# Kernel optimization log

Measured on AMD Instinct MI355X. Metric: run time of the kernel, lower is better.

The kernel has to match this reference:

```python
import jax, jax.numpy as jnp
import numpy as np

N = 50000        # nodes
E = 800000       # edges (avg degree 16)
IN = 128         # n_feat
C0, H0 = 32, 4   # layer0: out_channels, heads (concat -> 128)
C1, H1 = 32, 1   # layer1: out_channels, heads (mean)
NEG_SLOPE = 0.2


def setup_inputs() -> dict:
    key = jax.random.key(0)
    ks = jax.random.split(key, 16)
    def p(k, shape, fan):
        return jax.random.normal(k, shape, jnp.float32) / np.float32(np.sqrt(fan))
    x = jax.random.normal(ks[0], (N, IN), jnp.float32)
    edge_index = jax.random.randint(ks[1], (2, E), 0, N, dtype=jnp.int32)
    return {
        "x": x,
        "edge_index": edge_index,
        # layer 0 GATConv: in=128 -> 4 heads x 32, concat
        "W0": p(ks[2], (H0 * C0, IN), IN),
        "att_src0": p(ks[3], (H0, C0), C0),
        "att_dst0": p(ks[4], (H0, C0), C0),
        "bias0": jnp.zeros((H0 * C0,), jnp.float32),
        "linW0": p(ks[5], (H0 * C0, IN), IN),
        "linb0": jnp.zeros((H0 * C0,), jnp.float32),
        # layer 1 GATConv: in=128 -> 1 head x 32, mean
        "W1": p(ks[6], (H1 * C1, H0 * C0), H0 * C0),
        "att_src1": p(ks[7], (H1, C1), C1),
        "att_dst1": p(ks[8], (H1, C1), C1),
        "bias1": jnp.zeros((C1,), jnp.float32),
        "linW1": p(ks[9], (C1, H0 * C0), H0 * C0),
        "linb1": jnp.zeros((C1,), jnp.float32),
    }


def gat_conv(x, src, dst, W, att_src, att_dst, bias, concat):
    """PyG-style GATConv (self-loops already appended to src/dst)."""
    n = x.shape[0]
    H, C = att_src.shape
    h = (x @ W.T).reshape(n, H, C)                       # [N,H,C]
    a_src = jnp.einsum('nhc,hc->nh', h, att_src)          # [N,H]
    a_dst = jnp.einsum('nhc,hc->nh', h, att_dst)          # [N,H]
    e = jax.nn.leaky_relu(a_src[src] + a_dst[dst], NEG_SLOPE)  # [E,H]
    # segment softmax over incoming edges of each dst node
    m = jax.ops.segment_max(e, dst, num_segments=n)       # [N,H]
    ex = jnp.exp(e - m[dst])
    denom = jax.ops.segment_sum(ex, dst, num_segments=n)  # [N,H]
    alpha = ex / (denom[dst] + 1e-16)                     # [E,H]
    out = jax.ops.segment_sum(h[src] * alpha[:, :, None], dst, num_segments=n)  # [N,H,C]
    out = out.reshape(n, H * C) if concat else out.mean(axis=1)
    return out + bias


def reference(x, edge_index, W0, att_src0, att_dst0, bias0, linW0, linb0,
              W1, att_src1, att_dst1, bias1, linW1, linb1):
    n = x.shape[0]
    loop = jnp.arange(n, dtype=edge_index.dtype)
    src = jnp.concatenate([edge_index[0], loop])  # add self-loops
    dst = jnp.concatenate([edge_index[1], loop])
    # layer 0: conv + linear skip, then ELU (eval mode -> dropout is a no-op)
    h = gat_conv(x, src, dst, W0, att_src0, att_dst0, bias0, True) + x @ linW0.T + linb0
    h = jax.nn.elu(h)
    # layer 1 (last): conv + linear skip, no activation
    out = gat_conv(h, src, dst, W1, att_src1, att_dst1, bias1, False) + h @ linW1.T + linb1
    return out
```

## Files before the change

### kernel.cpp

```cpp
#include <hip/hip_runtime.h>
#include <hip/hip_bf16.h>


typedef __attribute__((ext_vector_type(8))) short bf8_t;
typedef __attribute__((ext_vector_type(4))) float f4_t;
typedef __attribute__((ext_vector_type(2))) float f2_t;

#define NBUCK 256
#define BCAP  8192

__device__ inline short f2bf(float f) {
    return (short)__builtin_bit_cast(unsigned short, __float2bfloat16(f));
}
__device__ inline float blo(unsigned int p) { return __uint_as_float(p << 16); }
__device__ inline float bhi(unsigned int p) { return __uint_as_float(p & 0xffff0000u); }
__device__ inline float lrexp(float e) {
    e = (e > 0.f) ? e : 0.2f * e;
    return __expf(e);
}

__global__ __launch_bounds__(256) void k_initbucket(
    const int* __restrict__ ei,
    const float* __restrict__ W0, const float* __restrict__ lW0,
    const float* __restrict__ W1, const float* __restrict__ lW1,
    const float* __restrict__ b0, const float* __restrict__ lb0,
    const float* __restrict__ b1, const float* __restrict__ lb1,
    short* __restrict__ Wp0, short* __restrict__ lWp0,
    short* __restrict__ Wp1, short* __restrict__ lWp1,
    float* __restrict__ bc0, float* __restrict__ bc1,
    int* __restrict__ gcur,
    unsigned int* __restrict__ bucketed, int E, int T) {
    __shared__ int hist[NBUCK];
    __shared__ int gbase[NBUCK];
    int tid = threadIdx.x;

    if (blockIdx.x < 64) {
        int i = blockIdx.x * 256 + tid;
        {
            int j = i & 7, lane = (i >> 3) & 63, kc = i >> 9;
            int kb = kc & 3, ct = kc >> 2;
            int src = (ct * 16 + (lane & 15)) * 128 + kb * 32 + (lane >> 4) * 8 + j;
            Wp0[i]  = f2bf(W0[src]);
            lWp0[i] = f2bf(lW0[src]);
            if (i < 4096) {
                Wp1[i]  = f2bf(W1[src]);
                lWp1[i] = f2bf(lW1[src]);
            }
        }
        if (i < 128) bc0[i] = b0[i] + lb0[i];
        else if (i < 160) bc1[i - 128] = b1[i - 128] + lb1[i - 128];
        return;
    }

    int bb = blockIdx.x - 64;
    hist[tid] = 0;
    __syncthreads();
    int base = bb * 2048;
    unsigned int pk[8]; int rk[8]; int bk[8];
    #pragma unroll
    for (int j = 0; j < 8; j++) {
        int e = base + j * 256 + tid;
        if (e < T) {
            int src, dst;
            if (e < E) { src = ei[e]; dst = ei[E + e]; }
            else       { src = e - E; dst = src; }
            int b = dst >> 8;
            pk[j] = ((unsigned int)dst << 16) | (unsigned int)src;
            bk[j] = b;
            rk[j] = atomicAdd(&hist[b], 1);
        } else bk[j] = -1;
    }
    __syncthreads();
    int h = hist[tid];
    if (h > 0) gbase[tid] = tid * BCAP + atomicAdd(&gcur[tid], h);
    __syncthreads();
    #pragma unroll
    for (int j = 0; j < 8; j++)
        if (bk[j] >= 0)
            bucketed[gbase[bk[j]] + rk[j]] = pk[j];
}


#define TSTR 136

__global__ __launch_bounds__(256) void k_fillgemm0(
    const unsigned int* __restrict__ bucketed, const int* __restrict__ gcur,
    int* __restrict__ rowstart,
    unsigned short* __restrict__ esrc,
    const float* __restrict__ x,
    const short* __restrict__ Wp0, const short* __restrict__ lWp0,
    const float* __restrict__ as0, const float* __restrict__ ad0,
    unsigned char* __restrict__ h0f8, __hip_bfloat16* __restrict__ skipb,
    float* __restrict__ a0s, float* __restrict__ a0d, int N) {
    __shared__ int ihist[256];
    __shared__ int incl[256];
    __shared__ short tile[4][16 * TSTR];
    __shared__ unsigned char t8[4][16 * 136];
    int NBK = (N + 255) >> 8;

    if ((int)blockIdx.x < NBK) {
        int b = blockIdx.x, t = threadIdx.x;
        int nodebase = b << 8;
        int cntt = gcur[t];
        incl[t] = cntt;
        __syncthreads();
        for (int off = 1; off < 256; off <<= 1) {
            int tv = (t >= off) ? incl[t - off] : 0;
            __syncthreads();
            incl[t] += tv;
            __syncthreads();
        }
        int rbase = (b > 0) ? incl[b - 1] : 0;
        if (b == 0 && t == 255) rowstart[N] = incl[255];
        int used = gcur[b];
        const unsigned int* bk = bucketed + (size_t)b * BCAP;
        __syncthreads();
        ihist[t] = 0;
        __syncthreads();
        for (int i = t; i < used; i += 256)
            atomicAdd(&ihist[(bk[i] >> 16) - nodebase], 1);
        __syncthreads();
        int v = ihist[t];
        incl[t] = v;
        __syncthreads();
        for (int off = 1; off < 256; off <<= 1) {
            int tv = (t >= off) ? incl[t - off] : 0;
            __syncthreads();
            incl[t] += tv;
            __syncthreads();
        }
        int myexcl = incl[t] - v;
        int node = nodebase + t;
        if (node < N) rowstart[node] = rbase + myexcl;
        __syncthreads();
        ihist[t] = myexcl;
        __syncthreads();
        for (int i = t; i < used; i += 256) {
            unsigned int p = bk[i];
            int pos = atomicAdd(&ihist[(p >> 16) - nodebase], 1);
            esrc[rbase + pos] = (unsigned short)(p & 0xffffu);
        }
        return;
    }

    int bx = blockIdx.x - NBK;
    int wv = threadIdx.x >> 6, lane = threadIdx.x & 63;
    int rowbase = bx * 64 + wv * 16;
    int m = lane & 15, q = lane >> 4;
    int arow = rowbase + m; if (arow >= N) arow = N - 1;
    bf8_t a[4];
    #pragma unroll
    for (int kb = 0; kb < 4; kb++) {
        const float4* px = (const float4*)(x + (size_t)arow * 128 + kb * 32 + q * 8);
        float4 lo = px[0], hi = px[1];
        bf8_t f;
        f[0] = f2bf(lo.x); f[1] = f2bf(lo.y); f[2] = f2bf(lo.z); f[3] = f2bf(lo.w);
        f[4] = f2bf(hi.x); f[5] = f2bf(hi.y); f[6] = f2bf(hi.z); f[7] = f2bf(hi.w);
        a[kb] = f;
    }
    float sacc[4][4], dacc[4][4];
    #pragma unroll
    for (int h = 0; h < 4; h++)
        #pragma unroll
        for (int r = 0; r < 4; r++) { sacc[h][r] = 0.f; dacc[h][r] = 0.f; }
    short* tl = tile[wv];
    unsigned char* t8l = t8[wv];
    int r4 = lane >> 2, qt = lane & 3;
    int drow = rowbase + r4;

    #pragma unroll
    for (int ct = 0; ct < 8; ct++) {
        f4_t acc = {0.f, 0.f, 0.f, 0.f};
        #pragma unroll
        for (int kb = 0; kb < 4; kb++) {
            bf8_t b = *(const bf8_t*)(Wp0 + (((ct * 4 + kb) * 64 + lane) << 3));
            acc = __builtin_amdgcn_mfma_f32_16x16x32_bf16(a[kb], b, acc, 0, 0, 0);
        }
        int hd = ct >> 1;
        float ws = as0[ct * 16 + m], wd = ad0[ct * 16 + m];
        #pragma unroll
        for (int r = 0; r < 4; r++) {
            sacc[hd][r] += acc[r] * ws;
            dacc[hd][r] += acc[r] * wd;
            int pk8 = __builtin_amdgcn_cvt_pk_fp8_f32(acc[r], acc[r], 0, false);
            t8l[(q * 4 + r) * 136 + ct * 16 + m] = (unsigned char)(pk8 & 0xff);
        }
    }
    if (drow < N) {
        const unsigned char* sp8 = t8l + r4 * 136 + qt * 32;
        uint2 w0 = ((const uint2*)sp8)[0];
        uint2 w1 = ((const uint2*)sp8)[1];
        uint2 w2 = ((const uint2*)sp8)[2];
        uint2 w3 = ((const uint2*)sp8)[3];
        uint4 o0 = make_uint4(w0.x, w0.y, w1.x, w1.y);
        uint4 o1 = make_uint4(w2.x, w2.y, w3.x, w3.y);
        unsigned char* dst = h0f8 + (size_t)drow * 128 + qt * 32;
        *(uint4*)dst = o0;
        *(uint4*)(dst + 16) = o1;
    }

    #pragma unroll
    for (int ct = 0; ct < 8; ct++) {
        f4_t acc = {0.f, 0.f, 0.f, 0.f};
        #pragma unroll
        for (int kb = 0; kb < 4; kb++) {
            bf8_t b = *(const bf8_t*)(lWp0 + (((ct * 4 + kb) * 64 + lane) << 3));
            acc = __builtin_amdgcn_mfma_f32_16x16x32_bf16(a[kb], b, acc, 0, 0, 0);
        }
        #pragma unroll
        for (int r = 0; r < 4; r++)
            tl[(q * 4 + r) * TSTR + ct * 16 + m] = f2bf(acc[r]);
    }
    if (drow < N) {
        short* dst = (short*)skipb + (size_t)drow * 128 + qt * 32;
        const short* srcp = tl + r4 * TSTR + qt * 32;
        #pragma unroll
        for (int s = 0; s < 4; s++)
            *(uint4*)(dst + s * 8) = *(const uint4*)(srcp + s * 8);
    }

    #pragma unroll
    for (int h = 0; h < 4; h++)
        #pragma unroll
        for (int r = 0; r < 4; r++) {
            float s = sacc[h][r], d = dacc[h][r];
            #pragma unroll
            for (int off = 1; off < 16; off <<= 1) {
                s += __shfl_xor(s, off);
                d += __shfl_xor(d, off);
            }
            sacc[h][r] = s; dacc[h][r] = d;
        }
    if (m < 4) {
        #pragma unroll
        for (int r = 0; r < 4; r++) {
            int row = rowbase + q * 4 + r;
            if (row < N) {
                float sv = (m == 0) ? sacc[0][r] : (m == 1) ? sacc[1][r]
                         : (m == 2) ? sacc[2][r] : sacc[3][r];
                float dv = (m == 0) ? dacc[0][r] : (m == 1) ? dacc[1][r]
                         : (m == 2) ? dacc[2][r] : dacc[3][r];
                a0s[row * 4 + m] = sv;
                a0d[row * 4 + m] = dv;
            }
        }
    }
}


__global__ __launch_bounds__(256) void k_aggfuse(
    const int* __restrict__ rowstart, const unsigned short* __restrict__ esrc,
    const uint2* __restrict__ h0f8,
    const float* __restrict__ a0s, const float* __restrict__ a0d,
    const float* __restrict__ bc0,
    const unsigned int* __restrict__ skip0,
    const short* __restrict__ Wp1, const short* __restrict__ lWp1,
    const float* __restrict__ as1, const float* __restrict__ ad1,
    __hip_bfloat16* __restrict__ h1, float* __restrict__ outskip,
    float* __restrict__ a1s, float* __restrict__ a1d, int n) {
    __shared__ __align__(16) short hrow[16][136];
    __shared__ __align__(16) short th[16 * 40];
    __shared__ __align__(16) float ts[16 * 36];
    __shared__ float satt[2][16], datt[2][16];

    int tid = threadIdx.x;
    int nl = tid >> 4, t = tid & 15, hd = t >> 2;
    int rowbase = blockIdx.x << 4;
    int node = rowbase + nl;

    if (node < n) {
        float ad = a0d[node * 4 + hd];
        int s0 = rowstart[node], s1 = rowstart[node + 1];
        float den = 0.f;
        float acc[8];
        #pragma unroll
        for (int k = 0; k < 8; k++) acc[k] = 0.f;
        int i = s0;
        for (; i + 3 < s1; i += 4) {
            int sE[4]; float e[4]; uint2 p[4];
            #pragma unroll
            for (int j = 0; j < 4; j++) sE[j] = esrc[i + j];
            #pragma unroll
            for (int j = 0; j < 4; j++) e[j] = a0s[sE[j] * 4 + hd] + ad;
            #pragma unroll
            for (int j = 0; j < 4; j++) p[j] = h0f8[(size_t)sE[j] * 16 + t];
            #pragma unroll
            for (int j = 0; j < 4; j++) {
                float wgt = lrexp(e[j]);
                den += wgt;
                f2_t c01 = __builtin_amdgcn_cvt_pk_f32_fp8(p[j].x, false);
                f2_t c23 = __builtin_amdgcn_cvt_pk_f32_fp8(p[j].x, true);
                f2_t c45 = __builtin_amdgcn_cvt_pk_f32_fp8(p[j].y, false);
                f2_t c67 = __builtin_amdgcn_cvt_pk_f32_fp8(p[j].y, true);
                acc[0] += wgt * c01.x; acc[1] += wgt * c01.y;
                acc[2] += wgt * c23.x; acc[3] += wgt * c23.y;
                acc[4] += wgt * c45.x; acc[5] += wgt * c45.y;
                acc[6] += wgt * c67.x; acc[7] += wgt * c67.y;
            }
        }
        for (; i < s1; ++i) {
            int s = esrc[i];
            float wgt = lrexp(a0s[s * 4 + hd] + ad);
            uint2 p = h0f8[(size_t)s * 16 + t];
            den += wgt;
            f2_t c01 = __builtin_amdgcn_cvt_pk_f32_fp8(p.x, false);
            f2_t c23 = __builtin_amdgcn_cvt_pk_f32_fp8(p.x, true);
            f2_t c45 = __builtin_amdgcn_cvt_pk_f32_fp8(p.y, false);
            f2_t c67 = __builtin_amdgcn_cvt_pk_f32_fp8(p.y, true);
            acc[0] += wgt * c01.x; acc[1] += wgt * c01.y;
            acc[2] += wgt * c23.x; acc[3] += wgt * c23.y;
            acc[4] += wgt * c45.x; acc[5] += wgt * c45.y;
            acc[6] += wgt * c67.x; acc[7] += wgt * c67.y;
        }
        float inv = 1.0f / (den + 1e-16f);
        uint4 sp = *(const uint4*)(skip0 + (size_t)node * 64 + t * 4);
        int c0 = t * 8;
        float o[8];
        o[0] = acc[0] * inv + blo(sp.x) + bc0[c0 + 0];
        o[1] = acc[1] * inv + bhi(sp.x) + bc0[c0 + 1];
        o[2] = acc[2] * inv + blo(sp.y) + bc0[c0 + 2];
        o[3] = acc[3] * inv + bhi(sp.y) + bc0[c0 + 3];
        o[4] = acc[4] * inv + blo(sp.z) + bc0[c0 + 4];
        o[5] = acc[5] * inv + bhi(sp.z) + bc0[c0 + 5];
        o[6] = acc[6] * inv + blo(sp.w) + bc0[c0 + 6];
        o[7] = acc[7] * inv + bhi(sp.w) + bc0[c0 + 7];
        #pragma unroll
        for (int k = 0; k < 8; k++)
            o[k] = (o[k] > 0.f) ? o[k] : (__expf(o[k]) - 1.f);
        uint4 res;
        res.x = (unsigned int)(unsigned short)f2bf(o[0]) | ((unsigned int)(unsigned short)f2bf(o[1]) << 16);
        res.y = (unsigned int)(unsigned short)f2bf(o[2]) | ((unsigned int)(unsigned short)f2bf(o[3]) << 16);
        res.z = (unsigned int)(unsigned short)f2bf(o[4]) | ((unsigned int)(unsigned short)f2bf(o[5]) << 16);
        res.w = (unsigned int)(unsigned short)f2bf(o[6]) | ((unsigned int)(unsigned short)f2bf(o[7]) << 16);
        *(uint4*)&hrow[nl][t * 8] = res;
    } else {
        *(uint4*)&hrow[nl][t * 8] = make_uint4(0u, 0u, 0u, 0u);
    }
    __syncthreads();

    int wv = tid >> 6, lane = tid & 63;
    int m = lane & 15, q = lane >> 4;
    bf8_t a[4];
    #pragma unroll
    for (int kb = 0; kb < 4; kb++)
        a[kb] = *(const bf8_t*)&hrow[m][kb * 32 + q * 8];
    int ct = wv & 1;
    const short* Wt = (wv < 2) ? Wp1 : lWp1;
    f4_t acc = {0.f, 0.f, 0.f, 0.f};
    #pragma unroll
    for (int kb = 0; kb < 4; kb++) {
        bf8_t b = *(const bf8_t*)(Wt + (((ct * 4 + kb) * 64 + lane) << 3));
        acc = __builtin_amdgcn_mfma_f32_16x16x32_bf16(a[kb], b, acc, 0, 0, 0);
    }
    if (wv < 2) {
        float wsv = as1[ct * 16 + m], wdv = ad1[ct * 16 + m];
        #pragma unroll
        for (int r = 0; r < 4; r++) {
            th[(q * 4 + r) * 40 + ct * 16 + m] = f2bf(acc[r]);
            float s = acc[r] * wsv, d = acc[r] * wdv;
            #pragma unroll
            for (int off = 1; off < 16; off <<= 1) {
                s += __shfl_xor(s, off);
                d += __shfl_xor(d, off);
            }
            if (m == 0) { satt[ct][q * 4 + r] = s; datt[ct][q * 4 + r] = d; }
        }
    } else {
        #pragma unroll
        for (int r = 0; r < 4; r++)
            ts[(q * 4 + r) * 36 + ct * 16 + m] = acc[r];
    }
    __syncthreads();

    if (tid < 64) {
        int row = tid >> 2, qt = tid & 3;
        if (rowbase + row < n)
            *(uint4*)((short*)h1 + (size_t)(rowbase + row) * 32 + qt * 8) =
                *(const uint4*)&th[row * 40 + qt * 8];
    } else if (tid < 192) {
        int i2 = tid - 64, row = i2 >> 3, qt = i2 & 7;
        if (rowbase + row < n)
            *(uint4*)(outskip + (size_t)(rowbase + row) * 32 + qt * 4) =
                *(const uint4*)&ts[row * 36 + qt * 4];
    } else if (tid < 208) {
        int r2 = tid - 192;
        if (rowbase + r2 < n) {
            a1s[rowbase + r2] = satt[0][r2] + satt[1][r2];
            a1d[rowbase + r2] = datt[0][r2] + datt[1][r2];
        }
    }
}


__global__ __launch_bounds__(256) void k_agg1(
    const int* __restrict__ rowstart, const unsigned short* __restrict__ esrc,
    const __hip_bfloat16* __restrict__ h1,
    const float* __restrict__ a1s, const float* __restrict__ a1d,
    const float* __restrict__ bc1,
    float* __restrict__ out, int n) {
    int node = (blockIdx.x * 256 + threadIdx.x) >> 6;
    int lane = threadIdx.x & 63;
    if (node >= n) return;
    int g = lane >> 4, t = lane & 15;
    float ad = a1d[node];
    int s0 = rowstart[node], s1 = rowstart[node + 1];
    const unsigned int* h1w = (const unsigned int*)h1;
    float den = 0.f, acc0 = 0.f, acc1 = 0.f;
    int i = s0 + g;
    for (; i + 12 < s1; i += 16) {
        int sE[4]; float e[4]; unsigned int p[4];
        #pragma unroll
        for (int j = 0; j < 4; j++) sE[j] = esrc[i + 4 * j];
        #pragma unroll
        for (int j = 0; j < 4; j++) e[j] = a1s[sE[j]] + ad;
        #pragma unroll
        for (int j = 0; j < 4; j++) p[j] = h1w[(size_t)sE[j] * 16 + t];
        #pragma unroll
        for (int j = 0; j < 4; j++) {
            float wgt = lrexp(e[j]);
            den += wgt;
            acc0 += wgt * blo(p[j]);
            acc1 += wgt * bhi(p[j]);
        }
    }
    for (; i < s1; i += 4) {
        int s = esrc[i];
        float wv = lrexp(a1s[s] + ad);
        unsigned int p = h1w[(size_t)s * 16 + t];
        den += wv; acc0 += wv * blo(p); acc1 += wv * bhi(p);
    }
    acc0 += __shfl_xor(acc0, 16); acc0 += __shfl_xor(acc0, 32);
    acc1 += __shfl_xor(acc1, 16); acc1 += __shfl_xor(acc1, 32);
    den  += __shfl_xor(den, 16);  den  += __shfl_xor(den, 32);
    if (g == 0) {
        float inv = 1.0f / (den + 1e-16f);
        int c0 = t * 2;
        size_t idx = (size_t)node * 32 + c0;
        float2 sk = *(const float2*)(out + idx);
        float2 r;
        r.x = acc0 * inv + sk.x + bc1[c0];
        r.y = acc1 * inv + sk.y + bc1[c0 + 1];
        *(float2*)(out + idx) = r;
    }
}


extern "C" void kernel_launch(void* const* d_in, const int* in_sizes, int n_in,
                              void* d_out, int out_size, void* d_ws, size_t ws_size,
                              hipStream_t stream) {
    const float* x   = (const float*)d_in[0];
    const int*   ei  = (const int*)d_in[1];
    const float* W0  = (const float*)d_in[2];
    const float* as0 = (const float*)d_in[3];
    const float* ad0 = (const float*)d_in[4];
    const float* b0  = (const float*)d_in[5];
    const float* lW0 = (const float*)d_in[6];
    const float* lb0 = (const float*)d_in[7];
    const float* W1  = (const float*)d_in[8];
    const float* as1 = (const float*)d_in[9];
    const float* ad1 = (const float*)d_in[10];
    const float* b1  = (const float*)d_in[11];
    const float* lW1 = (const float*)d_in[12];
    const float* lb1 = (const float*)d_in[13];
    float* out = (float*)d_out;

    const int N = in_sizes[0] / 128;
    const int E = in_sizes[1] / 2;
    const int T = E + N;
    const int NBK  = (N + 255) >> 8;
    const int NBBK = (T + 2047) / 2048;

    char* w = (char*)d_ws;
    auto alloc = [&](size_t bytes) -> char* {
        char* p = w; w += (bytes + 255) / 256 * 256; return p;
    };
    int* rowstart  = (int*)alloc((size_t)(N + 1) * 4);
    int* gcur      = (int*)alloc(NBUCK * 4);
    unsigned int* bucketed = (unsigned int*)alloc((size_t)NBUCK * BCAP * 4);
    unsigned short* esrc = (unsigned short*)alloc((size_t)T * 2);
    float* aS      = (float*)alloc((size_t)N * 4 * 4);
    float* aD      = (float*)alloc((size_t)N * 4 * 4);
    char* hbuf     = alloc((size_t)N * 128);
    __hip_bfloat16* skip0 = (__hip_bfloat16*)alloc((size_t)N * 128 * 2);
    __hip_bfloat16* h1buf = (__hip_bfloat16*)alloc((size_t)N * 32 * 2);
    float* aS1     = (float*)alloc((size_t)N * 4);
    float* aD1     = (float*)alloc((size_t)N * 4);
    short* Wp0  = (short*)alloc(16384 * 2);
    short* lWp0 = (short*)alloc(16384 * 2);
    short* Wp1  = (short*)alloc(4096 * 2);
    short* lWp1 = (short*)alloc(4096 * 2);
    float* bc0  = (float*)alloc(128 * 4);
    float* bc1  = (float*)alloc(32 * 4);

    hipMemsetAsync(gcur, 0, NBUCK * sizeof(int), stream);
    k_initbucket<<<64 + NBBK, 256, 0, stream>>>(ei, W0, lW0, W1, lW1,
                                                b0, lb0, b1, lb1,
                                                Wp0, lWp0, Wp1, lWp1, bc0, bc1,
                                                gcur, bucketed, E, T);
    k_fillgemm0<<<NBK + (N + 63) / 64, 256, 0, stream>>>(
        bucketed, gcur, rowstart, esrc,
        x, Wp0, lWp0, as0, ad0, (unsigned char*)hbuf, skip0, aS, aD, N);
    k_aggfuse<<<(N + 15) / 16, 256, 0, stream>>>(
        rowstart, esrc, (const uint2*)hbuf, aS, aD, bc0,
        (const unsigned int*)skip0, Wp1, lWp1, as1, ad1,
        h1buf, out, aS1, aD1, N);
    k_agg1<<<(N + 3) / 4, 256, 0, stream>>>(rowstart, esrc, h1buf,
                                            aS1, aD1, bc1, out, N);
}
```

Baseline: 187.6 us.

## Merge four kernels and memset into one persistent cooperative kernel with grid syncs

Replaces the memset plus four separate kernel launches with a single cooperative persistent kernel. The blocks loop over virtual block indices for each stage and use grid.sync between stages. Shared memory is overlaid in one raw buffer. The goal is to remove launch overhead and inter-kernel gaps. The cost is lower occupancy, grid-sync barriers and a grid sized by occupancy queries.

```diff
diff --git a/kernel.cpp b/kernel.cpp
--- a/kernel.cpp
+++ b/kernel.cpp
@@ -1,5 +1,8 @@
 #include <hip/hip_runtime.h>
 #include <hip/hip_bf16.h>
+#include <hip/hip_cooperative_groups.h>
+
+namespace cg = cooperative_groups;
 
 
 typedef __attribute__((ext_vector_type(8))) short bf8_t;
@@ -8,6 +11,7 @@
 
 #define NBUCK 256
 #define BCAP  8192
+#define TSTR  136
 
 __device__ inline short f2bf(float f) {
     return (short)__builtin_bit_cast(unsigned short, __float2bfloat16(f));
@@ -19,491 +23,488 @@
     return __expf(e);
 }
 
-__global__ __launch_bounds__(256) void k_initbucket(
-    const int* __restrict__ ei,
-    const float* __restrict__ W0, const float* __restrict__ lW0,
-    const float* __restrict__ W1, const float* __restrict__ lW1,
-    const float* __restrict__ b0, const float* __restrict__ lb0,
-    const float* __restrict__ b1, const float* __restrict__ lb1,
-    short* __restrict__ Wp0, short* __restrict__ lWp0,
-    short* __restrict__ Wp1, short* __restrict__ lWp1,
-    float* __restrict__ bc0, float* __restrict__ bc1,
-    int* __restrict__ gcur,
-    unsigned int* __restrict__ bucketed, int E, int T) {
-    __shared__ int hist[NBUCK];
-    __shared__ int gbase[NBUCK];
-    int tid = threadIdx.x;
-
-    if (blockIdx.x < 64) {
-        int i = blockIdx.x * 256 + tid;
-        {
-            int j = i & 7, lane = (i >> 3) & 63, kc = i >> 9;
-            int kb = kc & 3, ct = kc >> 2;
-            int src = (ct * 16 + (lane & 15)) * 128 + kb * 32 + (lane >> 4) * 8 + j;
-            Wp0[i]  = f2bf(W0[src]);
-            lWp0[i] = f2bf(lW0[src]);
-            if (i < 4096) {
-                Wp1[i]  = f2bf(W1[src]);
-                lWp1[i] = f2bf(lW1[src]);
-            }
-        }
-        if (i < 128) bc0[i] = b0[i] + lb0[i];
-        else if (i < 160) bc1[i - 128] = b1[i - 128] + lb1[i - 128];
-        return;
-    }
-
-    int bb = blockIdx.x - 64;
-    hist[tid] = 0;
-    __syncthreads();
-    int base = bb * 2048;
-    unsigned int pk[8]; int rk[8]; int bk[8];
-    #pragma unroll
-    for (int j = 0; j < 8; j++) {
-        int e = base + j * 256 + tid;
-        if (e < T) {
-            int src, dst;
-            if (e < E) { src = ei[e]; dst = ei[E + e]; }
-            else       { src = e - E; dst = src; }
-            int b = dst >> 8;
-            pk[j] = ((unsigned int)dst << 16) | (unsigned int)src;
-            bk[j] = b;
-            rk[j] = atomicAdd(&hist[b], 1);
-        } else bk[j] = -1;
-    }
-    __syncthreads();
-    int h = hist[tid];
-    if (h > 0) gbase[tid] = tid * BCAP + atomicAdd(&gcur[tid], h);
-    __syncthreads();
-    #pragma unroll
-    for (int j = 0; j < 8; j++)
-        if (bk[j] >= 0)
-            bucketed[gbase[bk[j]] + rk[j]] = pk[j];
-}
-
-
-#define TSTR 136
-
-__global__ __launch_bounds__(256) void k_fillgemm0(
-    const unsigned int* __restrict__ bucketed, const int* __restrict__ gcur,
-    int* __restrict__ rowstart,
-    unsigned short* __restrict__ esrc,
-    const float* __restrict__ x,
-    const short* __restrict__ Wp0, const short* __restrict__ lWp0,
-    const float* __restrict__ as0, const float* __restrict__ ad0,
-    unsigned char* __restrict__ h0f8, __hip_bfloat16* __restrict__ skipb,
-    float* __restrict__ a0s, float* __restrict__ a0d, int N) {
-    __shared__ int ihist[256];
-    __shared__ int incl[256];
-    __shared__ short tile[4][16 * TSTR];
-    __shared__ unsigned char t8[4][16 * 136];
-    int NBK = (N + 255) >> 8;
-
-    if ((int)blockIdx.x < NBK) {
-        int b = blockIdx.x, t = threadIdx.x;
-        int nodebase = b << 8;
-        int cntt = gcur[t];
-        incl[t] = cntt;
-        __syncthreads();
-        for (int off = 1; off < 256; off <<= 1) {
-            int tv = (t >= off) ? incl[t - off] : 0;
-            __syncthreads();
-            incl[t] += tv;
-            __syncthreads();
-        }
-        int rbase = (b > 0) ? incl[b - 1] : 0;
-        if (b == 0 && t == 255) rowstart[N] = incl[255];
-        int used = gcur[b];
-        const unsigned int* bk = bucketed + (size_t)b * BCAP;
-        __syncthreads();
-        ihist[t] = 0;
-        __syncthreads();
-        for (int i = t; i < used; i += 256)
-            atomicAdd(&ihist[(bk[i] >> 16) - nodebase], 1);
-        __syncthreads();
-        int v = ihist[t];
-        incl[t] = v;
-        __syncthreads();
-        for (int off = 1; off < 256; off <<= 1) {
-            int tv = (t >= off) ? incl[t - off] : 0;
-            __syncthreads();
-            incl[t] += tv;
-            __syncthreads();
-        }
-        int myexcl = incl[t] - v;
-        int node = nodebase + t;
-        if (node < N) rowstart[node] = rbase + myexcl;
-        __syncthreads();
-        ihist[t] = myexcl;
-        __syncthreads();
-        for (int i = t; i < used; i += 256) {
-            unsigned int p = bk[i];
-            int pos = atomicAdd(&ihist[(p >> 16) - nodebase], 1);
-            esrc[rbase + pos] = (unsigned short)(p & 0xffffu);
-        }
-        return;
-    }
-
-    int bx = blockIdx.x - NBK;
-    int wv = threadIdx.x >> 6, lane = threadIdx.x & 63;
-    int rowbase = bx * 64 + wv * 16;
-    int m = lane & 15, q = lane >> 4;
-    int arow = rowbase + m; if (arow >= N) arow = N - 1;
-    bf8_t a[4];
-    #pragma unroll
-    for (int kb = 0; kb < 4; kb++) {
-        const float4* px = (const float4*)(x + (size_t)arow * 128 + kb * 32 + q * 8);
-        float4 lo = px[0], hi = px[1];
-        bf8_t f;
-        f[0] = f2bf(lo.x); f[1] = f2bf(lo.y); f[2] = f2bf(lo.z); f[3] = f2bf(lo.w);
-        f[4] = f2bf(hi.x); f[5] = f2bf(hi.y); f[6] = f2bf(hi.z); f[7] = f2bf(hi.w);
-        a[kb] = f;
-    }
-    float sacc[4][4], dacc[4][4];
-    #pragma unroll
-    for (int h = 0; h < 4; h++)
-        #pragma unroll
-        for (int r = 0; r < 4; r++) { sacc[h][r] = 0.f; dacc[h][r] = 0.f; }
-    short* tl = tile[wv];
-    unsigned char* t8l = t8[wv];
-    int r4 = lane >> 2, qt = lane & 3;
-    int drow = rowbase + r4;
-
-    #pragma unroll
-    for (int ct = 0; ct < 8; ct++) {
-        f4_t acc = {0.f, 0.f, 0.f, 0.f};
-        #pragma unroll
-        for (int kb = 0; kb < 4; kb++) {
-            bf8_t b = *(const bf8_t*)(Wp0 + (((ct * 4 + kb) * 64 + lane) << 3));
-            acc = __builtin_amdgcn_mfma_f32_16x16x32_bf16(a[kb], b, acc, 0, 0, 0);
-        }
-        int hd = ct >> 1;
-        float ws = as0[ct * 16 + m], wd = ad0[ct * 16 + m];
-        #pragma unroll
-        for (int r = 0; r < 4; r++) {
-            sacc[hd][r] += acc[r] * ws;
-            dacc[hd][r] += acc[r] * wd;
-            int pk8 = __builtin_amdgcn_cvt_pk_fp8_f32(acc[r], acc[r], 0, false);
-            t8l[(q * 4 + r) * 136 + ct * 16 + m] = (unsigned char)(pk8 & 0xff);
+struct GP {
+    const int* ei;
+    const float *x, *W0, *as0, *ad0, *b0, *lW0, *lb0;
+    const float *W1, *as1, *ad1, *b1, *lW1, *lb1;
+    float* out;
+    int* rowstart; int* gcur;
+    unsigned int* bucketed; unsigned short* esrc;
+    float *aS, *aD;
+    unsigned char* h0f8;
+    unsigned int* skip0u;
+    __hip_bfloat16* h1buf;
+    float *aS1, *aD1;
+    short *Wp0, *lWp0, *Wp1, *lWp1;
+    float *bc0, *bc1;
+    int N, E, T, NBBK, NBK, NG0, NAGF, NAG1;
+};
+
+__global__ __launch_bounds__(256, 4) void k_all(GP p) {
+    cg::grid_group grid = cg::this_grid();
+    __shared__ __align__(16) char Lraw[26112];
+    const int tid = threadIdx.x;
+    const int nblk = gridDim.x;
+
+    if (blockIdx.x == 0) p.gcur[tid] = 0;
+    __threadfence();
+    grid.sync();
+
+    for (int vb = blockIdx.x; vb < 64 + p.NBBK; vb += nblk) {
+        if (vb < 64) {
+            int i = vb * 256 + tid;
+            {
+                int j = i & 7, lane = (i >> 3) & 63, kc = i >> 9;
+                int kb = kc & 3, ct = kc >> 2;
+                int src = (ct * 16 + (lane & 15)) * 128 + kb * 32 + (lane >> 4) * 8 + j;
+                p.Wp0[i]  = f2bf(p.W0[src]);
+                p.lWp0[i] = f2bf(p.lW0[src]);
+                if (i < 4096) {
+                    p.Wp1[i]  = f2bf(p.W1[src]);
+                    p.lWp1[i] = f2bf(p.lW1[src]);
+                }
+            }
+            if (i < 128) p.bc0[i] = p.b0[i] + p.lb0[i];
+            else if (i < 160) p.bc1[i - 128] = p.b1[i - 128] + p.lb1[i - 128];
+        } else {
+            int* hist  = (int*)Lraw;
+            int* gbase = hist + NBUCK;
+            int bb = vb - 64;
+            hist[tid] = 0;
+            __syncthreads();
+            int base = bb * 2048;
+            unsigned int pk[8]; int rk[8]; int bk[8];
+            #pragma unroll
+            for (int j = 0; j < 8; j++) {
+                int e = base + j * 256 + tid;
+                if (e < p.T) {
+                    int src, dst;
+                    if (e < p.E) { src = p.ei[e]; dst = p.ei[p.E + e]; }
+                    else         { src = e - p.E; dst = src; }
+                    int b = dst >> 8;
+                    pk[j] = ((unsigned int)dst << 16) | (unsigned int)src;
+                    bk[j] = b;
+                    rk[j] = atomicAdd(&hist[b], 1);
+                } else bk[j] = -1;
+            }
+            __syncthreads();
+            int h = hist[tid];
+            if (h > 0) gbase[tid] = tid * BCAP + atomicAdd(&p.gcur[tid], h);
+            __syncthreads();
+            #pragma unroll
+            for (int j = 0; j < 8; j++)
+                if (bk[j] >= 0)
+                    p.bucketed[gbase[bk[j]] + rk[j]] = pk[j];
         }
     }
-    if (drow < N) {
-        const unsigned char* sp8 = t8l + r4 * 136 + qt * 32;
-        uint2 w0 = ((const uint2*)sp8)[0];
-        uint2 w1 = ((const uint2*)sp8)[1];
-        uint2 w2 = ((const uint2*)sp8)[2];
-        uint2 w3 = ((const uint2*)sp8)[3];
-        uint4 o0 = make_uint4(w0.x, w0.y, w1.x, w1.y);
-        uint4 o1 = make_uint4(w2.x, w2.y, w3.x, w3.y);
-        unsigned char* dst = h0f8 + (size_t)drow * 128 + qt * 32;
-        *(uint4*)dst = o0;
-        *(uint4*)(dst + 16) = o1;
+    __threadfence();
+    grid.sync();
+
+    for (int vb = blockIdx.x; vb < p.NBK + p.NG0; vb += nblk) {
+        __syncthreads();
+        if (vb < p.NBK) {
+            int* ihist = (int*)Lraw;
+            int* incl  = ihist + 256;
+            int b = vb, t = tid;
+            int nodebase = b << 8;
+            int cntt = p.gcur[t];
+            incl[t] = cntt;
+            __syncthreads();
+            for (int off = 1; off < 256; off <<= 1) {
+                int tv = (t >= off) ? incl[t - off] : 0;
+                __syncthreads();
+                incl[t] += tv;
+                __syncthreads();
+            }
+            int rbase = (b > 0) ? incl[b - 1] : 0;
+            if (b == 0 && t == 255) p.rowstart[p.N] = incl[255];
+            int used = p.gcur[b];
+            const unsigned int* bk = p.bucketed + (size_t)b * BCAP;
+            __syncthreads();
+            ihist[t] = 0;
+            __syncthreads();
+            for (int i = t; i < used; i += 256)
+                atomicAdd(&ihist[(bk[i] >> 16) - nodebase], 1);
+            __syncthreads();
+            int v = ihist[t];
+            incl[t] = v;
+            __syncthreads();
+            for (int off = 1; off < 256; off <<= 1) {
+                int tv = (t >= off) ? incl[t - off] : 0;
+                __syncthreads();
+                incl[t] += tv;
+                __syncthreads();
+            }
+            int myexcl = incl[t] - v;
+            int node = nodebase + t;
+            if (node < p.N) p.rowstart[node] = rbase + myexcl;
+            __syncthreads();
+            ihist[t] = myexcl;
+            __syncthreads();
+            for (int i = t; i < used; i += 256) {
+                unsigned int pkv = bk[i];
+                int pos = atomicAdd(&ihist[(pkv >> 16) - nodebase], 1);
+                p.esrc[rbase + pos] = (unsigned short)(pkv & 0xffffu);
+            }
+        } else {
+            int bx = vb - p.NBK;
+            int wv = tid >> 6, lane = tid & 63;
+            int rowbase = bx * 64 + wv * 16;
+            int m = lane & 15, q = lane >> 4;
+            int arow = rowbase + m; if (arow >= p.N) arow = p.N - 1;
+            bf8_t a[4];
+            #pragma unroll
+            for (int kb = 0; kb < 4; kb++) {
+                const float4* px = (const float4*)(p.x + (size_t)arow * 128 + kb * 32 + q * 8);
+                float4 lo = px[0], hi = px[1];
+                bf8_t f;
+                f[0] = f2bf(lo.x); f[1] = f2bf(lo.y); f[2] = f2bf(lo.z); f[3] = f2bf(lo.w);
+                f[4] = f2bf(hi.x); f[5] = f2bf(hi.y); f[6] = f2bf(hi.z); f[7] = f2bf(hi.w);
+                a[kb] = f;
+            }
+            float sacc[4][4], dacc[4][4];
+            #pragma unroll
+            for (int h = 0; h < 4; h++)
+                #pragma unroll
+                for (int r = 0; r < 4; r++) { sacc[h][r] = 0.f; dacc[h][r] = 0.f; }
+            short* tl = (short*)Lraw + wv * 16 * TSTR;
+            unsigned char* t8l = (unsigned char*)(Lraw + 17408) + wv * 16 * 136;
+            int r4 = lane >> 2, qt = lane & 3;
+            int drow = rowbase + r4;
+
+            #pragma unroll
+            for (int ct = 0; ct < 8; ct++) {
+                f4_t acc = {0.f, 0.f, 0.f, 0.f};
+                #pragma unroll
+                for (int kb = 0; kb < 4; kb++) {
+                    bf8_t b = *(const bf8_t*)(p.Wp0 + (((ct * 4 + kb) * 64 + lane) << 3));
+                    acc = __builtin_amdgcn_mfma_f32_16x16x32_bf16(a[kb], b, acc, 0, 0, 0);
+                }
+                int hd = ct >> 1;
+                float ws = p.as0[ct * 16 + m], wd = p.ad0[ct * 16 + m];
+                #pragma unroll
+                for (int r = 0; r < 4; r++) {
+                    sacc[hd][r] += acc[r] * ws;
+                    dacc[hd][r] += acc[r] * wd;
+                    int pk8 = __builtin_amdgcn_cvt_pk_fp8_f32(acc[r], acc[r], 0, false);
+                    t8l[(q * 4 + r) * 136 + ct * 16 + m] = (unsigned char)(pk8 & 0xff);
+                }
+            }
+            if (drow < p.N) {
+                const unsigned char* sp8 = t8l + r4 * 136 + qt * 32;
+                uint2 w0 = ((const uint2*)sp8)[0];
+                uint2 w1 = ((const uint2*)sp8)[1];
+                uint2 w2 = ((const uint2*)sp8)[2];
+                uint2 w3 = ((const uint2*)sp8)[3];
+                uint4 o0 = make_uint4(w0.x, w0.y, w1.x, w1.y);
+                uint4 o1 = make_uint4(w2.x, w2.y, w3.x, w3.y);
+                unsigned char* dst = p.h0f8 + (size_t)drow * 128 + qt * 32;
+                *(uint4*)dst = o0;
+                *(uint4*)(dst + 16) = o1;
+            }
+
+            #pragma unroll
+            for (int ct = 0; ct < 8; ct++) {
+                f4_t acc = {0.f, 0.f, 0.f, 0.f};
+                #pragma unroll
+                for (int kb = 0; kb < 4; kb++) {
+                    bf8_t b = *(const bf8_t*)(p.lWp0 + (((ct * 4 + kb) * 64 + lane) << 3));
+                    acc = __builtin_amdgcn_mfma_f32_16x16x32_bf16(a[kb], b, acc, 0, 0, 0);
+                }
+                #pragma unroll
+                for (int r = 0; r < 4; r++)
+                    tl[(q * 4 + r) * TSTR + ct * 16 + m] = f2bf(acc[r]);
+            }
+            if (drow < p.N) {
+                short* dst = (short*)p.skip0u + (size_t)drow * 128 + qt * 32;
+                const short* srcp = tl + r4 * TSTR + qt * 32;
+                #pragma unroll
+                for (int s = 0; s < 4; s++)
+                    *(uint4*)(dst + s * 8) = *(const uint4*)(srcp + s * 8);
+            }
+
+            #pragma unroll
+            for (int h = 0; h < 4; h++)
+                #pragma unroll
+                for (int r = 0; r < 4; r++) {
+                    float s = sacc[h][r], d = dacc[h][r];
+                    #pragma unroll
+                    for (int off = 1; off < 16; off <<= 1) {
+                        s += __shfl_xor(s, off);
+                        d += __shfl_xor(d, off);
+                    }
+                    sacc[h][r] = s; dacc[h][r] = d;
+                }
+            if (m < 4) {
+                #pragma unroll
+                for (int r = 0; r < 4; r++) {
+                    int row = rowbase + q * 4 + r;
+                    if (row < p.N) {
+                        float sv = (m == 0) ? sacc[0][r] : (m == 1) ? sacc[1][r]
+                                 : (m == 2) ? sacc[2][r] : sacc[3][r];
+                        float dv = (m == 0) ? dacc[0][r] : (m == 1) ? dacc[1][r]
+                                 : (m == 2) ? dacc[2][r] : dacc[3][r];
+                        p.aS[row * 4 + m] = sv;
+                        p.aD[row * 4 + m] = dv;
+                    }
+                }
+            }
+        }
     }
-
-    #pragma unroll
-    for (int ct = 0; ct < 8; ct++) {
-        f4_t acc = {0.f, 0.f, 0.f, 0.f};
-        #pragma unroll
-        for (int kb = 0; kb < 4; kb++) {
-            bf8_t b = *(const bf8_t*)(lWp0 + (((ct * 4 + kb) * 64 + lane) << 3));
-            acc = __builtin_amdgcn_mfma_f32_16x16x32_bf16(a[kb], b, acc, 0, 0, 0);
+    __threadfence();
+    grid.sync();
+
+    {
+        short* hrow = (short*)Lraw;
+        short* th   = (short*)(Lraw + 4352);
+        float* ts   = (float*)(Lraw + 5632);
+        float* satt = (float*)(Lraw + 7936);
+        float* datt = (float*)(Lraw + 8064);
+        const uint2* h0f8v = (const uint2*)p.h0f8;
+        for (int vb = blockIdx.x; vb < p.NAGF; vb += nblk) {
+            int nl = tid >> 4, t = tid & 15, hd = t >> 2;
+            int rowbase = vb << 4;
+            int node = rowbase + nl;
+            if (node < p.N) {
+                float ad = p.aD[node * 4 + hd];
+                int s0 = p.rowstart[node], s1 = p.rowstart[node + 1];
+                float den = 0.f;
+                float acc[8];
+                #pragma unroll
+                for (int k = 0; k < 8; k++) acc[k] = 0.f;
+                int i = s0;
+                for (; i + 3 < s1; i += 4) {
+                    int sE[4]; float e[4]; uint2 pw[4];
+                    #pragma unroll
+                    for (int j = 0; j < 4; j++) sE[j] = p.esrc[i + j];
+                    #pragma unroll
+                    for (int j = 0; j < 4; j++) e[j] = p.aS[sE[j] * 4 + hd] + ad;
+                    #pragma unroll
+                    for (int j = 0; j < 4; j++) pw[j] = h0f8v[(size_t)sE[j] * 16 + t];
+                    #pragma unroll
+                    for (int j = 0; j < 4; j++) {
+                        float wgt = lrexp(e[j]);
+                        den += wgt;
+                        f2_t c01 = __builtin_amdgcn_cvt_pk_f32_fp8(pw[j].x, false);
+                        f2_t c23 = __builtin_amdgcn_cvt_pk_f32_fp8(pw[j].x, true);
+                        f2_t c45 = __builtin_amdgcn_cvt_pk_f32_fp8(pw[j].y, false);
+                        f2_t c67 = __builtin_amdgcn_cvt_pk_f32_fp8(pw[j].y, true);
+                        acc[0] += wgt * c01.x; acc[1] += wgt * c01.y;
+                        acc[2] += wgt * c23.x; acc[3] += wgt * c23.y;
+                        acc[4] += wgt * c45.x; acc[5] += wgt * c45.y;
+                        acc[6] += wgt * c67.x; acc[7] += wgt * c67.y;
+                    }
+                }
+                for (; i < s1; ++i) {
+                    int s = p.esrc[i];
+                    float wgt = lrexp(p.aS[s * 4 + hd] + ad);
+                    uint2 pw = h0f8v[(size_t)s * 16 + t];
+                    den += wgt;
+                    f2_t c01 = __builtin_amdgcn_cvt_pk_f32_fp8(pw.x, false);
+                    f2_t c23 = __builtin_amdgcn_cvt_pk_f32_fp8(pw.x, true);
+                    f2_t c45 = __builtin_amdgcn_cvt_pk_f32_fp8(pw.y, false);
+                    f2_t c67 = __builtin_amdgcn_cvt_pk_f32_fp8(pw.y, true);
+                    acc[0] += wgt * c01.x; acc[1] += wgt * c01.y;
+                    acc[2] += wgt * c23.x; acc[3] += wgt * c23.y;
+                    acc[4] += wgt * c45.x; acc[5] += wgt * c45.y;
+                    acc[6] += wgt * c67.x; acc[7] += wgt * c67.y;
+                }
+                float inv = 1.0f / (den + 1e-16f);
+                uint4 sp = *(const uint4*)(p.skip0u + (size_t)node * 64 + t * 4);
+                int c0 = t * 8;
+                float o[8];
+                o[0] = acc[0] * inv + blo(sp.x) + p.bc0[c0 + 0];
+                o[1] = acc[1] * inv + bhi(sp.x) + p.bc0[c0 + 1];
+                o[2] = acc[2] * inv + blo(sp.y) + p.bc0[c0 + 2];
+                o[3] = acc[3] * inv + bhi(sp.y) + p.bc0[c0 + 3];
+                o[4] = acc[4] * inv + blo(sp.z) + p.bc0[c0 + 4];
+                o[5] = acc[5] * inv + bhi(sp.z) + p.bc0[c0 + 5];
+                o[6] = acc[6] * inv + blo(sp.w) + p.bc0[c0 + 6];
+                o[7] = acc[7] * inv + bhi(sp.w) + p.bc0[c0 + 7];
+                #pragma unroll
+                for (int k = 0; k < 8; k++)
+                    o[k] = (o[k] > 0.f) ? o[k] : (__expf(o[k]) - 1.f);
+                uint4 res;
+                res.x = (unsigned int)(unsigned short)f2bf(o[0]) | ((unsigned int)(unsigned short)f2bf(o[1]) << 16);
+                res.y = (unsigned int)(unsigned short)f2bf(o[2]) | ((unsigned int)(unsigned short)f2bf(o[3]) << 16);
+                res.z = (unsigned int)(unsigned short)f2bf(o[4]) | ((unsigned int)(unsigned short)f2bf(o[5]) << 16);
+                res.w = (unsigned int)(unsigned short)f2bf(o[6]) | ((unsigned int)(unsigned short)f2bf(o[7]) << 16);
+                *(uint4*)&hrow[nl * 136 + t * 8] = res;
+            } else {
+                *(uint4*)&hrow[nl * 136 + t * 8] = make_uint4(0u, 0u, 0u, 0u);
+            }
+            __syncthreads();
+
+            int wv = tid >> 6, lane = tid & 63;
+            int m = lane & 15, q = lane >> 4;
+            bf8_t a[4];
+            #pragma unroll
+            for (int kb = 0; kb < 4; kb++)
+                a[kb] = *(const bf8_t*)&hrow[m * 136 + kb * 32 + q * 8];
+            int ct = wv & 1;
+            const short* Wt = (wv < 2) ? p.Wp1 : p.lWp1;
+            f4_t acc2 = {0.f, 0.f, 0.f, 0.f};
+            #pragma unroll
+            for (int kb = 0; kb < 4; kb++) {
+                bf8_t b = *(const bf8_t*)(Wt + (((ct * 4 + kb) * 64 + lane) << 3));
+                acc2 = __builtin_amdgcn_mfma_f32_16x16x32_bf16(a[kb], b, acc2, 0, 0, 0);
+            }
+            if (wv < 2) {
+                float wsv = p.as1[ct * 16 + m], wdv = p.ad1[ct * 16 + m];
+                #pragma unroll
+                for (int r = 0; r < 4; r++) {
+                    th[(q * 4 + r) * 40 + ct * 16 + m] = f2bf(acc2[r]);
+                    float s = acc2[r] * wsv, d = acc2[r] * wdv;
+                    #pragma unroll
+                    for (int off = 1; off < 16; off <<= 1) {
+                        s += __shfl_xor(s, off);
+                        d += __shfl_xor(d, off);
+                    }
+                    if (m == 0) { satt[ct * 16 + q * 4 + r] = s; datt[ct * 16 + q * 4 + r] = d; }
+                }
+            } else {
+                #pragma unroll
+                for (int r = 0; r < 4; r++)
+                    ts[(q * 4 + r) * 36 + ct * 16 + m] = acc2[r];
+            }
+            __syncthreads();
+
+            if (tid < 64) {
+                int row = tid >> 2, qt = tid & 3;
+                if (rowbase + row < p.N)
+                    *(uint4*)((short*)p.h1buf + (size_t)(rowbase + row) * 32 + qt * 8) =
+                        *(const uint4*)&th[row * 40 + qt * 8];
+            } else if (tid < 192) {
+                int i2 = tid - 64, row = i2 >> 3, qt = i2 & 7;
+                if (rowbase + row < p.N)
+                    *(uint4*)(p.out + (size_t)(rowbase + row) * 32 + qt * 4) =
+                        *(const uint4*)&ts[row * 36 + qt * 4];
+            } else if (tid < 208) {
+                int r2 = tid - 192;
+                if (rowbase + r2 < p.N) {
+                    p.aS1[rowbase + r2] = satt[r2] + satt[16 + r2];
+                    p.aD1[rowbase + r2] = datt[r2] + datt[16 + r2];
+                }
+            }
+            __syncthreads();
         }
-        #pragma unroll
-        for (int r = 0; r < 4; r++)
-            tl[(q * 4 + r) * TSTR + ct * 16 + m] = f2bf(acc[r]);
     }
-    if (drow < N) {
-        short* dst = (short*)skipb + (size_t)drow * 128 + qt * 32;
-        const short* srcp = tl + r4 * TSTR + qt * 32;
-        #pragma unroll
-        for (int s = 0; s < 4; s++)
-            *(uint4*)(dst + s * 8) = *(const uint4*)(srcp + s * 8);
-    }
-
-    #pragma unroll
-    for (int h = 0; h < 4; h++)
-        #pragma unroll
-        for (int r = 0; r < 4; r++) {
-            float s = sacc[h][r], d = dacc[h][r];
-            #pragma unroll
-            for (int off = 1; off < 16; off <<= 1) {
-                s += __shfl_xor(s, off);
-                d += __shfl_xor(d, off);
-            }
-            sacc[h][r] = s; dacc[h][r] = d;
-        }
-    if (m < 4) {
-        #pragma unroll
-        for (int r = 0; r < 4; r++) {
-            int row = rowbase + q * 4 + r;
-            if (row < N) {
-                float sv = (m == 0) ? sacc[0][r] : (m == 1) ? sacc[1][r]
-                         : (m == 2) ? sacc[2][r] : sacc[3][r];
-                float dv = (m == 0) ? dacc[0][r] : (m == 1) ? dacc[1][r]
-                         : (m == 2) ? dacc[2][r] : dacc[3][r];
-                a0s[row * 4 + m] = sv;
-                a0d[row * 4 + m] = dv;
+    __threadfence();
+    grid.sync();
+
+    {
+        const unsigned int* h1w = (const unsigned int*)p.h1buf;
+        for (int vb = blockIdx.x; vb < p.NAG1; vb += nblk) {
+            int node = (vb * 256 + tid) >> 6;
+            int lane = tid & 63;
+            if (node >= p.N) continue;
+            int g = lane >> 4, t = lane & 15;
+            float ad = p.aD1[node];
+            int s0 = p.rowstart[node], s1 = p.rowstart[node + 1];
+            float den = 0.f, acc0 = 0.f, acc1 = 0.f;
+            int i = s0 + g;
+            for (; i + 12 < s1; i += 16) {
+                int sE[4]; float e[4]; unsigned int pw[4];
+                #pragma unroll
+                for (int j = 0; j < 4; j++) sE[j] = p.esrc[i + 4 * j];
+                #pragma unroll
+                for (int j = 0; j < 4; j++) e[j] = p.aS1[sE[j]] + ad;
+                #pragma unroll
+                for (int j = 0; j < 4; j++) pw[j] = h1w[(size_t)sE[j] * 16 + t];
+                #pragma unroll
+                for (int j = 0; j < 4; j++) {
+                    float wgt = lrexp(e[j]);
+                    den += wgt;
+                    acc0 += wgt * blo(pw[j]);
+                    acc1 += wgt * bhi(pw[j]);
+                }
+            }
+            for (; i < s1; i += 4) {
+                int s = p.esrc[i];
+                float wv2 = lrexp(p.aS1[s] + ad);
+                unsigned int pw = h1w[(size_t)s * 16 + t];
+                den += wv2; acc0 += wv2 * blo(pw); acc1 += wv2 * bhi(pw);
+            }
+            acc0 += __shfl_xor(acc0, 16); acc0 += __shfl_xor(acc0, 32);
+            acc1 += __shfl_xor(acc1, 16); acc1 += __shfl_xor(acc1, 32);
+            den  += __shfl_xor(den, 16);  den  += __shfl_xor(den, 32);
+            if (g == 0) {
+                float inv = 1.0f / (den + 1e-16f);
+                int c0 = t * 2;
+                size_t idx = (size_t)node * 32 + c0;
+                float2 sk = *(const float2*)(p.out + idx);
+                float2 r;
+                r.x = acc0 * inv + sk.x + p.bc1[c0];
+                r.y = acc1 * inv + sk.y + p.bc1[c0 + 1];
+                *(float2*)(p.out + idx) = r;
             }
         }
     }
 }
 
 
-__global__ __launch_bounds__(256) void k_aggfuse(
-    const int* __restrict__ rowstart, const unsigned short* __restrict__ esrc,
-    const uint2* __restrict__ h0f8,
-    const float* __restrict__ a0s, const float* __restrict__ a0d,
-    const float* __restrict__ bc0,
-    const unsigned int* __restrict__ skip0,
-    const short* __restrict__ Wp1, const short* __restrict__ lWp1,
-    const float* __restrict__ as1, const float* __restrict__ ad1,
-    __hip_bfloat16* __restrict__ h1, float* __restrict__ outskip,
-    float* __restrict__ a1s, float* __restrict__ a1d, int n) {
-    __shared__ __align__(16) short hrow[16][136];
-    __shared__ __align__(16) short th[16 * 40];
-    __shared__ __align__(16) float ts[16 * 36];
-    __shared__ float satt[2][16], datt[2][16];
-
-    int tid = threadIdx.x;
-    int nl = tid >> 4, t = tid & 15, hd = t >> 2;
-    int rowbase = blockIdx.x << 4;
-    int node = rowbase + nl;
-
-    if (node < n) {
-        float ad = a0d[node * 4 + hd];
-        int s0 = rowstart[node], s1 = rowstart[node + 1];
-        float den = 0.f;
-        float acc[8];
-        #pragma unroll
-        for (int k = 0; k < 8; k++) acc[k] = 0.f;
-        int i = s0;
-        for (; i + 3 < s1; i += 4) {
-            int sE[4]; float e[4]; uint2 p[4];
-            #pragma unroll
-            for (int j = 0; j < 4; j++) sE[j] = esrc[i + j];
-            #pragma unroll
-            for (int j = 0; j < 4; j++) e[j] = a0s[sE[j] * 4 + hd] + ad;
-            #pragma unroll
-            for (int j = 0; j < 4; j++) p[j] = h0f8[(size_t)sE[j] * 16 + t];
-            #pragma unroll
-            for (int j = 0; j < 4; j++) {
-                float wgt = lrexp(e[j]);
-                den += wgt;
-                f2_t c01 = __builtin_amdgcn_cvt_pk_f32_fp8(p[j].x, false);
-                f2_t c23 = __builtin_amdgcn_cvt_pk_f32_fp8(p[j].x, true);
-                f2_t c45 = __builtin_amdgcn_cvt_pk_f32_fp8(p[j].y, false);
-                f2_t c67 = __builtin_amdgcn_cvt_pk_f32_fp8(p[j].y, true);
-                acc[0] += wgt * c01.x; acc[1] += wgt * c01.y;
-                acc[2] += wgt * c23.x; acc[3] += wgt * c23.y;
-                acc[4] += wgt * c45.x; acc[5] += wgt * c45.y;
-                acc[6] += wgt * c67.x; acc[7] += wgt * c67.y;
-            }
-        }
-        for (; i < s1; ++i) {
-            int s = esrc[i];
-            float wgt = lrexp(a0s[s * 4 + hd] + ad);
-            uint2 p = h0f8[(size_t)s * 16 + t];
-            den += wgt;
-            f2_t c01 = __builtin_amdgcn_cvt_pk_f32_fp8(p.x, false);
-            f2_t c23 = __builtin_amdgcn_cvt_pk_f32_fp8(p.x, true);
-            f2_t c45 = __builtin_amdgcn_cvt_pk_f32_fp8(p.y, false);
-            f2_t c67 = __builtin_amdgcn_cvt_pk_f32_fp8(p.y, true);
-            acc[0] += wgt * c01.x; acc[1] += wgt * c01.y;
-            acc[2] += wgt * c23.x; acc[3] += wgt * c23.y;
-            acc[4] += wgt * c45.x; acc[5] += wgt * c45.y;
-            acc[6] += wgt * c67.x; acc[7] += wgt * c67.y;
-        }
-        float inv = 1.0f / (den + 1e-16f);
-        uint4 sp = *(const uint4*)(skip0 + (size_t)node * 64 + t * 4);
-        int c0 = t * 8;
-        float o[8];
-        o[0] = acc[0] * inv + blo(sp.x) + bc0[c0 + 0];
-        o[1] = acc[1] * inv + bhi(sp.x) + bc0[c0 + 1];
-        o[2] = acc[2] * inv + blo(sp.y) + bc0[c0 + 2];
-        o[3] = acc[3] * inv + bhi(sp.y) + bc0[c0 + 3];
-        o[4] = acc[4] * inv + blo(sp.z) + bc0[c0 + 4];
-        o[5] = acc[5] * inv + bhi(sp.z) + bc0[c0 + 5];
-        o[6] = acc[6] * inv + blo(sp.w) + bc0[c0 + 6];
-        o[7] = acc[7] * inv + bhi(sp.w) + bc0[c0 + 7];
-        #pragma unroll
-        for (int k = 0; k < 8; k++)
-            o[k] = (o[k] > 0.f) ? o[k] : (__expf(o[k]) - 1.f);
-        uint4 res;
-        res.x = (unsigned int)(unsigned short)f2bf(o[0]) | ((unsigned int)(unsigned short)f2bf(o[1]) << 16);
-        res.y = (unsigned int)(unsigned short)f2bf(o[2]) | ((unsigned int)(unsigned short)f2bf(o[3]) << 16);
-        res.z = (unsigned int)(unsigned short)f2bf(o[4]) | ((unsigned int)(unsigned short)f2bf(o[5]) << 16);
-        res.w = (unsigned int)(unsigned short)f2bf(o[6]) | ((unsigned int)(unsigned short)f2bf(o[7]) << 16);
-        *(uint4*)&hrow[nl][t * 8] = res;
-    } else {
-        *(uint4*)&hrow[nl][t * 8] = make_uint4(0u, 0u, 0u, 0u);
-    }
-    __syncthreads();
-
-    int wv = tid >> 6, lane = tid & 63;
-    int m = lane & 15, q = lane >> 4;
-    bf8_t a[4];
-    #pragma unroll
-    for (int kb = 0; kb < 4; kb++)
-        a[kb] = *(const bf8_t*)&hrow[m][kb * 32 + q * 8];
-    int ct = wv & 1;
-    const short* Wt = (wv < 2) ? Wp1 : lWp1;
-    f4_t acc = {0.f, 0.f, 0.f, 0.f};
-    #pragma unroll
-    for (int kb = 0; kb < 4; kb++) {
-        bf8_t b = *(const bf8_t*)(Wt + (((ct * 4 + kb) * 64 + lane) << 3));
-        acc = __builtin_amdgcn_mfma_f32_16x16x32_bf16(a[kb], b, acc, 0, 0, 0);
-    }
-    if (wv < 2) {
-        float wsv = as1[ct * 16 + m], wdv = ad1[ct * 16 + m];
-        #pragma unroll
-        for (int r = 0; r < 4; r++) {
-            th[(q * 4 + r) * 40 + ct * 16 + m] = f2bf(acc[r]);
-            float s = acc[r] * wsv, d = acc[r] * wdv;
-            #pragma unroll
-            for (int off = 1; off < 16; off <<= 1) {
-                s += __shfl_xor(s, off);
-                d += __shfl_xor(d, off);
-            }
-            if (m == 0) { satt[ct][q * 4 + r] = s; datt[ct][q * 4 + r] = d; }
-        }
-    } else {
-        #pragma unroll
-        for (int r = 0; r < 4; r++)
-            ts[(q * 4 + r) * 36 + ct * 16 + m] = acc[r];
-    }
-    __syncthreads();
-
-    if (tid < 64) {
-        int row = tid >> 2, qt = tid & 3;
-        if (rowbase + row < n)
-            *(uint4*)((short*)h1 + (size_t)(rowbase + row) * 32 + qt * 8) =
-                *(const uint4*)&th[row * 40 + qt * 8];
-    } else if (tid < 192) {
-        int i2 = tid - 64, row = i2 >> 3, qt = i2 & 7;
-        if (rowbase + row < n)
-            *(uint4*)(outskip + (size_t)(rowbase + row) * 32 + qt * 4) =
-                *(const uint4*)&ts[row * 36 + qt * 4];
-    } else if (tid < 208) {
-        int r2 = tid - 192;
-        if (rowbase + r2 < n) {
-            a1s[rowbase + r2] = satt[0][r2] + satt[1][r2];
-            a1d[rowbase + r2] = datt[0][r2] + datt[1][r2];
-        }
-    }
-}
-
-
-__global__ __launch_bounds__(256) void k_agg1(
-    const int* __restrict__ rowstart, const unsigned short* __restrict__ esrc,
-    const __hip_bfloat16* __restrict__ h1,
-    const float* __restrict__ a1s, const float* __restrict__ a1d,
-    const float* __restrict__ bc1,
-    float* __restrict__ out, int n) {
-    int node = (blockIdx.x * 256 + threadIdx.x) >> 6;
-    int lane = threadIdx.x & 63;
-    if (node >= n) return;
-    int g = lane >> 4, t = lane & 15;
-    float ad = a1d[node];
-    int s0 = rowstart[node], s1 = rowstart[node + 1];
-    const unsigned int* h1w = (const unsigned int*)h1;
-    float den = 0.f, acc0 = 0.f, acc1 = 0.f;
-    int i = s0 + g;
-    for (; i + 12 < s1; i += 16) {
-        int sE[4]; float e[4]; unsigned int p[4];
-        #pragma unroll
-        for (int j = 0; j < 4; j++) sE[j] = esrc[i + 4 * j];
-        #pragma unroll
-        for (int j = 0; j < 4; j++) e[j] = a1s[sE[j]] + ad;
-        #pragma unroll
-        for (int j = 0; j < 4; j++) p[j] = h1w[(size_t)sE[j] * 16 + t];
-        #pragma unroll
-        for (int j = 0; j < 4; j++) {
-            float wgt = lrexp(e[j]);
-            den += wgt;
-            acc0 += wgt * blo(p[j]);
-            acc1 += wgt * bhi(p[j]);
-        }
-    }
-    for (; i < s1; i += 4) {
-        int s = esrc[i];
-        float wv = lrexp(a1s[s] + ad);
-        unsigned int p = h1w[(size_t)s * 16 + t];
-        den += wv; acc0 += wv * blo(p); acc1 += wv * bhi(p);
-    }
-    acc0 += __shfl_xor(acc0, 16); acc0 += __shfl_xor(acc0, 32);
-    acc1 += __shfl_xor(acc1, 16); acc1 += __shfl_xor(acc1, 32);
-    den  += __shfl_xor(den, 16);  den  += __shfl_xor(den, 32);
-    if (g == 0) {
-        float inv = 1.0f / (den + 1e-16f);
-        int c0 = t * 2;
-        size_t idx = (size_t)node * 32 + c0;
-        float2 sk = *(const float2*)(out + idx);
-        float2 r;
-        r.x = acc0 * inv + sk.x + bc1[c0];
-        r.y = acc1 * inv + sk.y + bc1[c0 + 1];
-        *(float2*)(out + idx) = r;
-    }
-}
-
-
 extern "C" void kernel_launch(void* const* d_in, const int* in_sizes, int n_in,
                               void* d_out, int out_size, void* d_ws, size_t ws_size,
                               hipStream_t stream) {
-    const float* x   = (const float*)d_in[0];
-    const int*   ei  = (const int*)d_in[1];
-    const float* W0  = (const float*)d_in[2];
-    const float* as0 = (const float*)d_in[3];
-    const float* ad0 = (const float*)d_in[4];
-    const float* b0  = (const float*)d_in[5];
-    const float* lW0 = (const float*)d_in[6];
-    const float* lb0 = (const float*)d_in[7];
-    const float* W1  = (const float*)d_in[8];
-    const float* as1 = (const float*)d_in[9];
-    const float* ad1 = (const float*)d_in[10];
-    const float* b1  = (const float*)d_in[11];
-    const float* lW1 = (const float*)d_in[12];
-    const float* lb1 = (const float*)d_in[13];
-    float* out = (float*)d_out;
-
     const int N = in_sizes[0] / 128;
     const int E = in_sizes[1] / 2;
     const int T = E + N;
-    const int NBK  = (N + 255) >> 8;
-    const int NBBK = (T + 2047) / 2048;
 
     char* w = (char*)d_ws;
     auto alloc = [&](size_t bytes) -> char* {
-        char* p = w; w += (bytes + 255) / 256 * 256; return p;
+        char* pp = w; w += (bytes + 255) / 256 * 256; return pp;
     };
-    int* rowstart  = (int*)alloc((size_t)(N + 1) * 4);
-    int* gcur      = (int*)alloc(NBUCK * 4);
-    unsigned int* bucketed = (unsigned int*)alloc((size_t)NBUCK * BCAP * 4);
-    unsigned short* esrc = (unsigned short*)alloc((size_t)T * 2);
-    float* aS      = (float*)alloc((size_t)N * 4 * 4);
-    float* aD      = (float*)alloc((size_t)N * 4 * 4);
-    char* hbuf     = alloc((size_t)N * 128);
-    __hip_bfloat16* skip0 = (__hip_bfloat16*)alloc((size_t)N * 128 * 2);
-    __hip_bfloat16* h1buf = (__hip_bfloat16*)alloc((size_t)N * 32 * 2);
-    float* aS1     = (float*)alloc((size_t)N * 4);
-    float* aD1     = (float*)alloc((size_t)N * 4);
-    short* Wp0  = (short*)alloc(16384 * 2);
-    short* lWp0 = (short*)alloc(16384 * 2);
-    short* Wp1  = (short*)alloc(4096 * 2);
-    short* lWp1 = (short*)alloc(4096 * 2);
-    float* bc0  = (float*)alloc(128 * 4);
-    float* bc1  = (float*)alloc(32 * 4);
-
-    hipMemsetAsync(gcur, 0, NBUCK * sizeof(int), stream);
-    k_initbucket<<<64 + NBBK, 256, 0, stream>>>(ei, W0, lW0, W1, lW1,
-                                                b0, lb0, b1, lb1,
-                                                Wp0, lWp0, Wp1, lWp1, bc0, bc1,
-                                                gcur, bucketed, E, T);
-    k_fillgemm0<<<NBK + (N + 63) / 64, 256, 0, stream>>>(
-        bucketed, gcur, rowstart, esrc,
-        x, Wp0, lWp0, as0, ad0, (unsigned char*)hbuf, skip0, aS, aD, N);
-    k_aggfuse<<<(N + 15) / 16, 256, 0, stream>>>(
-        rowstart, esrc, (const uint2*)hbuf, aS, aD, bc0,
-        (const unsigned int*)skip0, Wp1, lWp1, as1, ad1,
-        h1buf, out, aS1, aD1, N);
-    k_agg1<<<(N + 3) / 4, 256, 0, stream>>>(rowstart, esrc, h1buf,
-                                            aS1, aD1, bc1, out, N);
+    GP p;
+    p.ei  = (const int*)d_in[1];
+    p.x   = (const float*)d_in[0];
+    p.W0  = (const float*)d_in[2];
+    p.as0 = (const float*)d_in[3];
+    p.ad0 = (const float*)d_in[4];
+    p.b0  = (const float*)d_in[5];
+    p.lW0 = (const float*)d_in[6];
+    p.lb0 = (const float*)d_in[7];
+    p.W1  = (const float*)d_in[8];
+    p.as1 = (const float*)d_in[9];
+    p.ad1 = (const float*)d_in[10];
+    p.b1  = (const float*)d_in[11];
+    p.lW1 = (const float*)d_in[12];
+    p.lb1 = (const float*)d_in[13];
+    p.out = (float*)d_out;
+
+    p.rowstart = (int*)alloc((size_t)(N + 1) * 4);
+    p.gcur     = (int*)alloc(NBUCK * 4);
+    p.bucketed = (unsigned int*)alloc((size_t)NBUCK * BCAP * 4);
+    p.esrc     = (unsigned short*)alloc((size_t)T * 2);
+    p.aS       = (float*)alloc((size_t)N * 4 * 4);
+    p.aD       = (float*)alloc((size_t)N * 4 * 4);
+    p.h0f8     = (unsigned char*)alloc((size_t)N * 128);
+    p.skip0u   = (unsigned int*)alloc((size_t)N * 128 * 2);
+    p.h1buf    = (__hip_bfloat16*)alloc((size_t)N * 32 * 2);
+    p.aS1      = (float*)alloc((size_t)N * 4);
+    p.aD1      = (float*)alloc((size_t)N * 4);
+    p.Wp0      = (short*)alloc(16384 * 2);
+    p.lWp0     = (short*)alloc(16384 * 2);
+    p.Wp1      = (short*)alloc(4096 * 2);
+    p.lWp1     = (short*)alloc(4096 * 2);
+    p.bc0      = (float*)alloc(128 * 4);
+    p.bc1      = (float*)alloc(32 * 4);
+
+    p.N = N; p.E = E; p.T = T;
+    p.NBBK = (T + 2047) / 2048;
+    p.NBK  = (N + 255) >> 8;
+    p.NG0  = (N + 63) / 64;
+    p.NAGF = (N + 15) / 16;
+    p.NAG1 = (N + 3) / 4;
+
+    int nbpc = 0;
+    hipOccupancyMaxActiveBlocksPerMultiprocessor(&nbpc, k_all, 256, 0);
+    if (nbpc < 1) nbpc = 1;
+    int ncu = 256;
+    hipDeviceGetAttribute(&ncu, hipDeviceAttributeMultiprocessorCount, 0);
+    int grid = nbpc * ncu;
+    if (grid > 2048) grid = 2048;
+
+    void* args[] = { (void*)&p };
+    hipLaunchCooperativeKernel((const void*)k_all, dim3(grid), dim3(256),
+                               args, 0, stream);
 }
```

New measurement: 733.5 us. 3.91x slower.
